# Kernel tuning notes

Measured on AMD Instinct MI355X. Metric: run time of the kernel, lower is better.

Reference implementation:

```python
import jax, jax.numpy as jnp
import numpy as np
from jax import lax

B, S, C, H, T = 64, 256, 64, 512, 128  # batch, enc seq, coord_dims, hidden, target_len

def _lstm_step(Wih, Whh, b, h, c, xt):
    # PyTorch gate order: i, f, g, o
    g = xt @ Wih.T + h @ Whh.T + b
    i, f, gg, o = jnp.split(g, 4, axis=-1)
    i = jax.nn.sigmoid(i); f = jax.nn.sigmoid(f)
    gg = jnp.tanh(gg); o = jax.nn.sigmoid(o)
    c = f * c + i * gg
    h = o * jnp.tanh(c)
    return h, c

def _lstm_layer(x_seq, Wih, Whh, b):
    # x_seq: [B, S, D] -> outputs [B, S, H], final (h, c)
    Bsz = x_seq.shape[0]
    h0 = jnp.zeros((Bsz, Whh.shape[1]), x_seq.dtype)
    c0 = jnp.zeros_like(h0)
    def step(carry, xt):
        h, c = carry
        h, c = _lstm_step(Wih, Whh, b, h, c, xt)
        return (h, c), h
    (hT, cT), ys = lax.scan(step, (h0, c0), x_seq.swapaxes(0, 1))
    return ys.swapaxes(0, 1), hT, cT

def setup_inputs() -> dict:
    key = jax.random.key(0)
    ks = jax.random.split(key, 16)
    s = 1.0 / np.sqrt(H)
    def u(k, shape):
        return jax.random.uniform(k, shape, jnp.float32, -s, s)
    inp = {"x": jax.random.normal(ks[0], (B, S, C), jnp.float32), "target_len": T}
    inp["enc_Wih0"] = u(ks[1], (4 * H, C)); inp["enc_Whh0"] = u(ks[2], (4 * H, H)); inp["enc_b0"] = u(ks[3], (4 * H,))
    inp["enc_Wih1"] = u(ks[4], (4 * H, H)); inp["enc_Whh1"] = u(ks[5], (4 * H, H)); inp["enc_b1"] = u(ks[6], (4 * H,))
    inp["dec_Wih0"] = u(ks[7], (4 * H, C)); inp["dec_Whh0"] = u(ks[8], (4 * H, H)); inp["dec_b0"] = u(ks[9], (4 * H,))
    inp["dec_Wih1"] = u(ks[10], (4 * H, H)); inp["dec_Whh1"] = u(ks[11], (4 * H, H)); inp["dec_b1"] = u(ks[12], (4 * H,))
    inp["lin_W"] = u(ks[13], (C, H)); inp["lin_b"] = u(ks[14], (C,))
    return inp

def reference(x, enc_Wih0, enc_Whh0, enc_b0, enc_Wih1, enc_Whh1, enc_b1,
              dec_Wih0, dec_Whh0, dec_b0, dec_Wih1, dec_Whh1, dec_b1,
              lin_W, lin_b, target_len):
    # ---- encoder: 2-layer LSTM over full sequence ----
    y0, h0, c0 = _lstm_layer(x, enc_Wih0, enc_Whh0, enc_b0)
    _, h1, c1 = _lstm_layer(y0, enc_Wih1, enc_Whh1, enc_b1)
    dec_in0 = x[:, -1, :]  # [B, C]
    def step(carry, _):
        xin, h0_, c0_, h1_, c1_ = carry
        h0n, c0n = _lstm_step(dec_Wih0, dec_Whh0, dec_b0, h0_, c0_, xin)
        h1n, c1n = _lstm_step(dec_Wih1, dec_Whh1, dec_b1, h1_, c1_, h0n)
        out = h1n @ lin_W.T + lin_b  # [B, C]
        return (out, h0n, c0n, h1n, c1n), out
    _, outs = lax.scan(step, (dec_in0, h0, c0, h1, c1), None, length=target_len)
    return outs.swapaxes(0, 1)  # [B, target_len, C]
```

## Files before the change

kernel.cpp:

```cpp
#include <hip/hip_runtime.h>

typedef _Float16 f16;
typedef _Float16 f16x4 __attribute__((ext_vector_type(4)));
typedef _Float16 f16x8 __attribute__((ext_vector_type(8)));
typedef float    f32x4 __attribute__((ext_vector_type(4)));

#define MFMA16(a,b,c) __builtin_amdgcn_mfma_f32_16x16x32_f16((a),(b),(c),0,0,0)

constexpr unsigned NB = 64, NS = 256, NC = 64, NH = 512, NT = 128;
constexpr unsigned HSLOT = NB * NH;

constexpr unsigned OFF_WX   = 0;
constexpr unsigned OFF_WLIN = OFF_WX   + NB*NS*NC*2;
constexpr unsigned OFF_EH0  = OFF_WLIN + NC*NH*2;
constexpr unsigned OFF_EH1  = OFF_EH0  + 2*HSLOT*2;
constexpr unsigned OFF_DH0  = OFF_EH1  + 2*HSLOT*2;
constexpr unsigned OFF_DH1  = OFF_DH0  + 2*HSLOT*2;
constexpr unsigned OFF_BAR  = OFF_DH1  + 2*HSLOT*2;


__global__ void prep_convert(const float* __restrict__ x,
                             const float* __restrict__ linw,
                             char* __restrict__ ws)
{
    unsigned rel = blockIdx.x * 256u + threadIdx.x;
    if (rel < 65536u) {
        unsigned t = rel >> 8, c4 = (rel >> 4) & 15u, b0 = (rel & 15u) << 2;
        #pragma unroll
        for (unsigned j = 0; j < 4; ++j) {
            float4 v = ((const float4*)x)[(b0 + j) * 4096u + t * 16u + c4];
            f16x4 o; o[0]=(f16)v.x; o[1]=(f16)v.y; o[2]=(f16)v.z; o[3]=(f16)v.w;
            ((f16x4*)(ws + OFF_WX))[t * 1024u + c4 * 64u + b0 + j] = o;
        }
    } else if ((rel -= 65536u) < 8192u) {
        float4 v = ((const float4*)linw)[rel];
        f16x4 o; o[0]=(f16)v.x; o[1]=(f16)v.y; o[2]=(f16)v.z; o[3]=(f16)v.w;
        ((f16x4*)(ws + OFF_WLIN))[rel] = o;
    } else if ((rel -= 8192u) < 32768u) {
        f16x8 z = {};
        ((f16x8*)(ws + OFF_EH0))[rel] = z;
    } else if ((rel -= 32768u) < 512u) {
        int4 z; z.x = z.y = z.z = z.w = 0;
        ((int4*)(ws + OFF_BAR))[rel] = z;
    }
}


__device__ __forceinline__ float sigm(float v)   { return 1.f / (1.f + __expf(-v)); }
__device__ __forceinline__ float tanh_f(float v) { return 2.f / (1.f + __expf(-2.f * v)) - 1.f; }

__device__ __forceinline__ void h_store8(f16* p, f16x4 v)
{
    union { unsigned long long u; f16x4 h; } c; c.h = v;
    __hip_atomic_store((unsigned long long*)p, c.u, __ATOMIC_RELAXED, __HIP_MEMORY_SCOPE_AGENT);
}
__device__ __forceinline__ f16x4 h_load8(const f16* p)
{
    unsigned long long v = __hip_atomic_load((const unsigned long long*)p,
                                             __ATOMIC_RELAXED, __HIP_MEMORY_SCOPE_AGENT);
    union { unsigned long long u; f16x4 h; } c; c.u = v;
    return c.h;
}
__device__ __forceinline__ f16x8 h_load_blk(const f16* slot, int kr, int m)
{
    const f16* p = slot + ((kr >> 2) << 8) + (m << 2);
    f16x4 a = h_load8(p);
    f16x4 b = h_load8(p + 256);
    f16x8 r;
    r[0]=a[0]; r[1]=a[1]; r[2]=a[2]; r[3]=a[3];
    r[4]=b[0]; r[5]=b[1]; r[6]=b[2]; r[7]=b[3];
    return r;
}

__device__ __forceinline__ void grid_barrier(int* bar, int wg, int tid, int& bgen)
{
    __syncthreads();
    if (tid == 0) {
        const int g = wg >> 4;
        int* grp   = bar + g * 32;
        int* root  = bar + 16 * 32;
        int* flags = bar + 17 * 32;
        const int target = bgen + 1;

        int old = __hip_atomic_fetch_add(grp, 1, __ATOMIC_RELAXED, __HIP_MEMORY_SCOPE_AGENT);
        if ((old & 15) == 15) {
            int ro = __hip_atomic_fetch_add(root, 1, __ATOMIC_RELAXED, __HIP_MEMORY_SCOPE_AGENT);
            if ((ro & 15) == 15) {
                #pragma unroll
                for (int i = 0; i < 16; ++i)
                    __hip_atomic_store(flags + i * 32, target, __ATOMIC_RELAXED, __HIP_MEMORY_SCOPE_AGENT);
            }
        }
        int* myf = flags + g * 32;
        while (__hip_atomic_load(myf, __ATOMIC_RELAXED, __HIP_MEMORY_SCOPE_AGENT) < target)
            __builtin_amdgcn_s_sleep(1);
        bgen = target;
    }
    __syncthreads();
}

__device__ __forceinline__ void load_wlds_f32(f16 (*Wlds)[1032],
                                              const float* __restrict__ A, int KA,
                                              const float* __restrict__ Bs, int KB,
                                              int u0, int tid)
{
    int nch = (KA + KB) >> 2;
    int tot = nch << 6;
    for (int idx = tid; idx < tot; idx += 256) {
        int j = idx / nch, ch = idx - j * nch;
        int k = ch << 2;
        int grow = ((j >> 4) << 9) + u0 + (j & 15);
        float4 v;
        if (k < KA) v = *(const float4*)(A + grow * KA + k);
        else        v = *(const float4*)(Bs + grow * KB + (k - KA));
        f16x4 o; o[0]=(f16)v.x; o[1]=(f16)v.y; o[2]=(f16)v.z; o[3]=(f16)v.w;
        *(f16x4*)&Wlds[j][k] = o;
    }
}

__device__ __forceinline__ void load_wlds_fold(f16 (*Wlds)[1032],
                                               const float* __restrict__ dwih0,
                                               const float* __restrict__ linw,
                                               const float* __restrict__ dwhh0,
                                               int u0, int tid)
{
    #pragma unroll
    for (int rep = 0; rep < 4; ++rep) {
        int idx = ((rep << 8) + tid) << 5;
        int j = idx >> 9, k0 = idx & 511;
        int grow = ((j >> 4) << 9) + u0 + (j & 15);
        float acc[32];
        #pragma unroll
        for (int q = 0; q < 32; ++q) acc[q] = 0.f;
        for (int c = 0; c < 64; ++c) {
            float wc = dwih0[grow * 64 + c];
            const float* lr = linw + c * 512 + k0;
            #pragma unroll
            for (int q = 0; q < 32; ++q) acc[q] += wc * lr[q];
        }
        #pragma unroll
        for (int q = 0; q < 32; ++q) Wlds[j][k0 + q] = (f16)acc[q];
    }
    int tot = 8192;
    for (int idx = tid; idx < tot; idx += 256) {
        int j = idx >> 7, ch = idx & 127, k = ch << 2;
        int grow = ((j >> 4) << 9) + u0 + (j & 15);
        float4 v = *(const float4*)(dwhh0 + grow * 512 + k);
        f16x4 o; o[0]=(f16)v.x; o[1]=(f16)v.y; o[2]=(f16)v.z; o[3]=(f16)v.w;
        *(f16x4*)&Wlds[j][512 + k] = o;
    }
}

template<int MAXS, bool EXACT>
__device__ __forceinline__ void rnn_round(f16 (*Wlds)[1032], float (*Dp)[16][68],
                                          const f16* __restrict__ A0, int K0,
                                          const f16* __restrict__ A1,
                                          int K, int kStart,
                                          const float* ba, float& creg,
                                          f16* __restrict__ ho,
                                          int u0, int b0, int tid)
{
    const int lane = tid & 63, wv = tid >> 6, q = lane >> 4, lo = lane & 15;
    const int sBeg = kStart >> 5, n = (K >> 5) - sBeg;
    const int per = n >> 2, rem = n & 3;
    const int s0 = sBeg + wv * per + (wv < rem ? wv : rem);
    const int ns = EXACT ? MAXS : (per + (wv < rem ? 1 : 0));

    int sEff[MAXS];
    #pragma unroll
    for (int s = 0; s < MAXS; ++s)
        sEff[s] = s0 + (EXACT ? s : (s < ns ? s : ns - 1));

    f16x8 A[MAXS];
    #pragma unroll
    for (int s = 0; s < MAXS; ++s) {
        int kb = sEff[s] << 5;
        bool in0 = kb < K0;
        const f16* src = in0 ? A0 : A1;
        int kr = (in0 ? kb : kb - K0) + (q << 3);
        A[s] = h_load_blk(src, kr, b0 + lo);
    }
    if (!EXACT) {
        if (MAXS - 1 >= ns) { f16x8 z = {}; A[MAXS-1] = z; }
    }
    __builtin_amdgcn_sched_barrier(0);

    f32x4 ac0 = {0.f,0.f,0.f,0.f}, ac1 = ac0, ac2 = ac0, ac3 = ac0;
    #pragma unroll
    for (int s = 0; s < MAXS; ++s) {
        int kk = (sEff[s] << 5) + (q << 3);
        ac0 = MFMA16(A[s], *(const f16x8*)&Wlds[lo     ][kk], ac0);
        ac1 = MFMA16(A[s], *(const f16x8*)&Wlds[lo + 16][kk], ac1);
        ac2 = MFMA16(A[s], *(const f16x8*)&Wlds[lo + 32][kk], ac2);
        ac3 = MFMA16(A[s], *(const f16x8*)&Wlds[lo + 48][kk], ac3);
    }

    #pragma unroll
    for (int r = 0; r < 4; ++r) {
        int rr = (q << 2) + r;
        Dp[wv][rr][lo     ] = ac0[r];
        Dp[wv][rr][lo + 16] = ac1[r];
        Dp[wv][rr][lo + 32] = ac2[r];
        Dp[wv][rr][lo + 48] = ac3[r];
    }
    __syncthreads();
    const int b = tid >> 4, u = tid & 15;
    float v[4];
    #pragma unroll
    for (int g = 0; g < 4; ++g) {
        int col = (g << 4) + u;
        v[g] = Dp[0][b][col] + Dp[1][b][col] + Dp[2][b][col] + Dp[3][b][col] + ba[g];
    }
    float ii = sigm(v[0]), ff = sigm(v[1]), gg = tanh_f(v[2]), oo = sigm(v[3]);
    creg = ff * creg + ii * gg;
    float h = oo * tanh_f(creg);
    float h1 = __shfl_down(h, 1);
    float h2 = __shfl_down(h, 2);
    float h3 = __shfl_down(h, 3);
    if ((u & 3) == 0) {
        f16x4 hv; hv[0] = (f16)h; hv[1] = (f16)h1; hv[2] = (f16)h2; hv[3] = (f16)h3;
        h_store8(ho + (((u0 + u) >> 2) << 8) + ((b0 + b) << 2), hv);
    }
}

__device__ __forceinline__ void out_gemm(const f16* __restrict__ H1,
                                         const f16* __restrict__ LW,
                                         const float* __restrict__ linb,
                                         float* __restrict__ out,
                                         int w, int t, int tid)
{
    const int lane = tid & 63, wv = tid >> 6, q = lane >> 4, lo = lane & 15;
    int b0 = w << 4;
    f32x4 ac = {0.f,0.f,0.f,0.f};
    int c0 = wv << 4;

    f16x8 a[16];
    #pragma unroll
    for (int s = 0; s < 16; ++s)
        a[s] = h_load_blk(H1, (s << 5) + (q << 3), b0 + lo);
    __builtin_amdgcn_sched_barrier(0);

    #pragma unroll
    for (int s = 0; s < 16; ++s) {
        int kk = (s << 5) + (q << 3);
        f16x8 bf = *(const f16x8*)(LW + (c0 + lo) * 512 + kk);
        ac = MFMA16(a[s], bf, ac);
    }
    float lb = linb[c0 + lo];
    #pragma unroll
    for (int r = 0; r < 4; ++r) {
        int b = b0 + (q << 2) + r;
        out[(size_t)b * (NT * NC) + t * NC + c0 + lo] = ac[r] + lb;
    }
}


__global__ void __launch_bounds__(256)
lstm_main(char* __restrict__ ws,
          const float* __restrict__ x,
          const float* __restrict__ wih0, const float* __restrict__ whh0, const float* __restrict__ eb0,
          const float* __restrict__ wih1, const float* __restrict__ whh1, const float* __restrict__ eb1,
          const float* __restrict__ dwih0, const float* __restrict__ dwhh0, const float* __restrict__ db0,
          const float* __restrict__ dwih1, const float* __restrict__ dwhh1, const float* __restrict__ db1,
          const float* __restrict__ linw, const float* __restrict__ linb,
          float* __restrict__ out)
{
    __shared__ f16   Wlds[64][1032];
    __shared__ float Dp[4][16][68];

    const int wg = blockIdx.x, tid = threadIdx.x;
    const bool isL0 = wg < 128;
    const int wl = wg & 127;
    const int b0 = (wl & 3) << 4;
    const int u0 = (wl >> 2) << 4;
    const int u  = tid & 15;
    int* bar = (int*)(ws + OFF_BAR);
    int bgen = 0;

    const f16* WX   = (const f16*)(ws + OFF_WX);
    const f16* WLIN = (const f16*)(ws + OFF_WLIN);
    f16* EH0 = (f16*)(ws + OFF_EH0);
    f16* EH1 = (f16*)(ws + OFF_EH1);
    f16* DH0 = (f16*)(ws + OFF_DH0);
    f16* DH1 = (f16*)(ws + OFF_DH1);

    if (isL0) load_wlds_f32(Wlds, wih0,  64, whh0, 512, u0, tid);
    else      load_wlds_f32(Wlds, wih1, 512, whh1, 512, u0, tid);
    __syncthreads();

    float ba[4];
    {
        const float* bs = isL0 ? eb0 : eb1;
        #pragma unroll
        for (int g = 0; g < 4; ++g) ba[g] = bs[(g << 9) + u0 + u];
    }
    float creg = 0.f;

    for (int r = 0; r <= (int)NS; ++r) {
        if (isL0 && r < (int)NS) {
            rnn_round<5,false>(Wlds, Dp,
                      WX + r * 4096, 64,
                      EH0 + ((r + 1) & 1) * HSLOT,
                      576, 0, ba, creg,
                      EH0 + (r & 1) * HSLOT, u0, b0, tid);
        } else if (!isL0 && r >= 1) {
            int t = r - 1;
            rnn_round<8,true>(Wlds, Dp,
                      EH0 + (t & 1) * HSLOT, 512,
                      EH1 + ((t + 1) & 1) * HSLOT,
                      1024, 0, ba, creg,
                      EH1 + (t & 1) * HSLOT, u0, b0, tid);
        }
        grid_barrier(bar, wg, tid, bgen);
    }

    float baI[4];
    if (isL0) {
        load_wlds_fold(Wlds, dwih0, linw, dwhh0, u0, tid);
        const int bb = b0 + (tid >> 4);
        const float* xr = x + bb * (NS * NC) + (NS - 1) * NC;
        #pragma unroll
        for (int g = 0; g < 4; ++g) {
            int row = (g << 9) + u0 + u;
            const float* wr = dwih0 + row * 64;
            float bsum = 0.f, xsum = 0.f;
            for (int c = 0; c < 64; ++c) { bsum += linb[c] * wr[c]; xsum += xr[c] * wr[c]; }
            ba[g]  = db0[row] + bsum;
            baI[g] = db0[row] + xsum;
        }
    } else {
        load_wlds_f32(Wlds, dwih1, 512, dwhh1, 512, u0, tid);
        #pragma unroll
        for (int g = 0; g < 4; ++g) { ba[g] = db1[(g << 9) + u0 + u]; baI[g] = 0.f; }
    }
    __syncthreads();

    for (int d = 0; d < 2 * (int)NT; ++d) {
        int t = d >> 1;
        if ((d & 1) == 0) {
            if (isL0) {
                if (t == 0) {
                    rnn_round<4,true>(Wlds, Dp, EH1 + HSLOT, 512, EH0 + HSLOT,
                              1024, 512, baI, creg,
                              DH0, u0, b0, tid);
                } else {
                    rnn_round<8,true>(Wlds, Dp,
                              DH1 + ((t + 1) & 1) * HSLOT, 512,
                              DH0 + ((t + 1) & 1) * HSLOT,
                              1024, 0, ba, creg,
                              DH0 + (t & 1) * HSLOT, u0, b0, tid);
                }
            } else if (wg < 132 && t >= 1) {
                out_gemm(DH1 + ((t - 1) & 1) * HSLOT, WLIN, linb, out, wg - 128, t - 1, tid);
            }
        } else {
            if (!isL0) {
                const f16* A1 = (t == 0) ? EH1 + HSLOT : DH1 + ((t + 1) & 1) * HSLOT;
                rnn_round<8,true>(Wlds, Dp,
                          DH0 + (t & 1) * HSLOT, 512,
                          A1, 1024, 0, ba, creg,
                          DH1 + (t & 1) * HSLOT, u0, b0, tid);
            }
        }
        grid_barrier(bar, wg, tid, bgen);
    }

    if (!isL0 && wg < 132)
        out_gemm(DH1 + HSLOT, WLIN, linb, out, wg - 128, (int)NT - 1, tid);
}


extern "C" void kernel_launch(void* const* d_in, const int* in_sizes, int n_in,
                              void* d_out, int out_size, void* d_ws, size_t ws_size,
                              hipStream_t stream)
{
    const float* x     = (const float*)d_in[0];
    const float* wih0  = (const float*)d_in[2];
    const float* whh0  = (const float*)d_in[3];
    const float* eb0   = (const float*)d_in[4];
    const float* wih1  = (const float*)d_in[5];
    const float* whh1  = (const float*)d_in[6];
    const float* eb1   = (const float*)d_in[7];
    const float* dwih0 = (const float*)d_in[8];
    const float* dwhh0 = (const float*)d_in[9];
    const float* db0   = (const float*)d_in[10];
    const float* dwih1 = (const float*)d_in[11];
    const float* dwhh1 = (const float*)d_in[12];
    const float* db1   = (const float*)d_in[13];
    const float* linw  = (const float*)d_in[14];
    const float* linb  = (const float*)d_in[15];
    char* ws    = (char*)d_ws;
    float* outp = (float*)d_out;

    prep_convert<<<418, 256, 0, stream>>>(x, linw, ws);

    lstm_main<<<256, 256, 0, stream>>>(ws, x, wih0, whh0, eb0, wih1, whh1, eb1,
                                       dwih0, dwhh0, db0, dwih1, dwhh1, db1,
                                       linw, linb, outp);
}
```

Before: 2.110 ms.

## Precompute recurrent-half GEMM during idle phase to shorten critical path

Each layer's workgroups now compute the half of the gate GEMM that depends on their own recurrent state (Whh·h) during the phase when they would otherwise idle. The partial accumulators are carried in registers to the next phase. That phase then only does the half that depends on the other layer's fresh output before the activation. This halves the MFMA work on the critical path between grid barriers. It costs extra register pressure and work in the previously idle phase, which for layer-1 groups now overlaps with the output GEMM.

```diff
diff --git a/kernel.cpp b/kernel.cpp
--- a/kernel.cpp
+++ b/kernel.cpp
@@ -151,50 +151,37 @@
     }
 }
 
-template<int MAXS, bool EXACT>
-__device__ __forceinline__ void rnn_round(f16 (*Wlds)[1032], float (*Dp)[16][68],
-                                          const f16* __restrict__ A0, int K0,
-                                          const f16* __restrict__ A1,
-                                          int K, int kStart,
-                                          const float* ba, float& creg,
-                                          f16* __restrict__ ho,
-                                          int u0, int b0, int tid)
+__device__ __forceinline__ void gemm_acc4(f16 (*Wlds)[1032],
+                                          const f16* __restrict__ A0, int kOff,
+                                          f32x4& ac0, f32x4& ac1, f32x4& ac2, f32x4& ac3,
+                                          int b0, int tid)
 {
     const int lane = tid & 63, wv = tid >> 6, q = lane >> 4, lo = lane & 15;
-    const int sBeg = kStart >> 5, n = (K >> 5) - sBeg;
-    const int per = n >> 2, rem = n & 3;
-    const int s0 = sBeg + wv * per + (wv < rem ? wv : rem);
-    const int ns = EXACT ? MAXS : (per + (wv < rem ? 1 : 0));
-
-    int sEff[MAXS];
-    #pragma unroll
-    for (int s = 0; s < MAXS; ++s)
-        sEff[s] = s0 + (EXACT ? s : (s < ns ? s : ns - 1));
-
-    f16x8 A[MAXS];
-    #pragma unroll
-    for (int s = 0; s < MAXS; ++s) {
-        int kb = sEff[s] << 5;
-        bool in0 = kb < K0;
-        const f16* src = in0 ? A0 : A1;
-        int kr = (in0 ? kb : kb - K0) + (q << 3);
-        A[s] = h_load_blk(src, kr, b0 + lo);
-    }
-    if (!EXACT) {
-        if (MAXS - 1 >= ns) { f16x8 z = {}; A[MAXS-1] = z; }
+    const int s0 = wv << 2;
+    f16x8 A[4];
+    #pragma unroll
+    for (int s = 0; s < 4; ++s) {
+        int kr = ((s0 + s) << 5) + (q << 3);
+        A[s] = h_load_blk(A0, kr, b0 + lo);
     }
     __builtin_amdgcn_sched_barrier(0);
-
-    f32x4 ac0 = {0.f,0.f,0.f,0.f}, ac1 = ac0, ac2 = ac0, ac3 = ac0;
-    #pragma unroll
-    for (int s = 0; s < MAXS; ++s) {
-        int kk = (sEff[s] << 5) + (q << 3);
+    #pragma unroll
+    for (int s = 0; s < 4; ++s) {
+        int kk = kOff + ((s0 + s) << 5) + (q << 3);
         ac0 = MFMA16(A[s], *(const f16x8*)&Wlds[lo     ][kk], ac0);
         ac1 = MFMA16(A[s], *(const f16x8*)&Wlds[lo + 16][kk], ac1);
         ac2 = MFMA16(A[s], *(const f16x8*)&Wlds[lo + 32][kk], ac2);
         ac3 = MFMA16(A[s], *(const f16x8*)&Wlds[lo + 48][kk], ac3);
     }
-
+}
+
+__device__ __forceinline__ void finish_round(float (*Dp)[16][68],
+                                             f32x4 ac0, f32x4 ac1, f32x4 ac2, f32x4 ac3,
+                                             const float* ba, float& creg,
+                                             f16* __restrict__ ho,
+                                             int u0, int b0, int tid)
+{
+    const int lane = tid & 63, wv = tid >> 6, q = lane >> 4, lo = lane & 15;
     #pragma unroll
     for (int r = 0; r < 4; ++r) {
         int rr = (q << 2) + r;
@@ -221,6 +208,52 @@
         f16x4 hv; hv[0] = (f16)h; hv[1] = (f16)h1; hv[2] = (f16)h2; hv[3] = (f16)h3;
         h_store8(ho + (((u0 + u) >> 2) << 8) + ((b0 + b) << 2), hv);
     }
+}
+
+template<int MAXS, bool EXACT>
+__device__ __forceinline__ void rnn_round(f16 (*Wlds)[1032], float (*Dp)[16][68],
+                                          const f16* __restrict__ A0, int K0,
+                                          const f16* __restrict__ A1,
+                                          int K, int kStart,
+                                          const float* ba, float& creg,
+                                          f16* __restrict__ ho,
+                                          int u0, int b0, int tid)
+{
+    const int lane = tid & 63, wv = tid >> 6, q = lane >> 4, lo = lane & 15;
+    const int sBeg = kStart >> 5, n = (K >> 5) - sBeg;
+    const int per = n >> 2, rem = n & 3;
+    const int s0 = sBeg + wv * per + (wv < rem ? wv : rem);
+    const int ns = EXACT ? MAXS : (per + (wv < rem ? 1 : 0));
+
+    int sEff[MAXS];
+    #pragma unroll
+    for (int s = 0; s < MAXS; ++s)
+        sEff[s] = s0 + (EXACT ? s : (s < ns ? s : ns - 1));
+
+    f16x8 A[MAXS];
+    #pragma unroll
+    for (int s = 0; s < MAXS; ++s) {
+        int kb = sEff[s] << 5;
+        bool in0 = kb < K0;
+        const f16* src = in0 ? A0 : A1;
+        int kr = (in0 ? kb : kb - K0) + (q << 3);
+        A[s] = h_load_blk(src, kr, b0 + lo);
+    }
+    if (!EXACT) {
+        if (MAXS - 1 >= ns) { f16x8 z = {}; A[MAXS-1] = z; }
+    }
+    __builtin_amdgcn_sched_barrier(0);
+
+    f32x4 ac0 = {0.f,0.f,0.f,0.f}, ac1 = ac0, ac2 = ac0, ac3 = ac0;
+    #pragma unroll
+    for (int s = 0; s < MAXS; ++s) {
+        int kk = (sEff[s] << 5) + (q << 3);
+        ac0 = MFMA16(A[s], *(const f16x8*)&Wlds[lo     ][kk], ac0);
+        ac1 = MFMA16(A[s], *(const f16x8*)&Wlds[lo + 16][kk], ac1);
+        ac2 = MFMA16(A[s], *(const f16x8*)&Wlds[lo + 32][kk], ac2);
+        ac3 = MFMA16(A[s], *(const f16x8*)&Wlds[lo + 48][kk], ac3);
+    }
+    finish_round(Dp, ac0, ac1, ac2, ac3, ba, creg, ho, u0, b0, tid);
 }
 
 __device__ __forceinline__ void out_gemm(const f16* __restrict__ H1,
@@ -335,31 +368,39 @@
     }
     __syncthreads();
 
+    f32x4 c0 = {0.f,0.f,0.f,0.f}, c1 = c0, c2 = c0, c3 = c0;
+    const f32x4 zero = {0.f,0.f,0.f,0.f};
+
     for (int d = 0; d < 2 * (int)NT; ++d) {
         int t = d >> 1;
         if ((d & 1) == 0) {
             if (isL0) {
                 if (t == 0) {
-                    rnn_round<4,true>(Wlds, Dp, EH1 + HSLOT, 512, EH0 + HSLOT,
-                              1024, 512, baI, creg,
-                              DH0, u0, b0, tid);
+                    f32x4 a0 = zero, a1 = zero, a2 = zero, a3 = zero;
+                    gemm_acc4(Wlds, EH0 + HSLOT, 512, a0, a1, a2, a3, b0, tid);
+                    finish_round(Dp, a0, a1, a2, a3, baI, creg, DH0, u0, b0, tid);
                 } else {
-                    rnn_round<8,true>(Wlds, Dp,
-                              DH1 + ((t + 1) & 1) * HSLOT, 512,
-                              DH0 + ((t + 1) & 1) * HSLOT,
-                              1024, 0, ba, creg,
-                              DH0 + (t & 1) * HSLOT, u0, b0, tid);
+                    f32x4 a0 = c0, a1 = c1, a2 = c2, a3 = c3;
+                    gemm_acc4(Wlds, DH1 + ((t + 1) & 1) * HSLOT, 0, a0, a1, a2, a3, b0, tid);
+                    finish_round(Dp, a0, a1, a2, a3, ba, creg,
+                                 DH0 + (t & 1) * HSLOT, u0, b0, tid);
                 }
-            } else if (wg < 132 && t >= 1) {
-                out_gemm(DH1 + ((t - 1) & 1) * HSLOT, WLIN, linb, out, wg - 128, t - 1, tid);
+            } else {
+                const f16* h1p = (t == 0) ? EH1 + HSLOT : DH1 + ((t + 1) & 1) * HSLOT;
+                c0 = zero; c1 = zero; c2 = zero; c3 = zero;
+                gemm_acc4(Wlds, h1p, 512, c0, c1, c2, c3, b0, tid);
+                if (wg < 132 && t >= 1)
+                    out_gemm(DH1 + ((t - 1) & 1) * HSLOT, WLIN, linb, out, wg - 128, t - 1, tid);
             }
         } else {
             if (!isL0) {
-                const f16* A1 = (t == 0) ? EH1 + HSLOT : DH1 + ((t + 1) & 1) * HSLOT;
-                rnn_round<8,true>(Wlds, Dp,
-                          DH0 + (t & 1) * HSLOT, 512,
-                          A1, 1024, 0, ba, creg,
-                          DH1 + (t & 1) * HSLOT, u0, b0, tid);
+                f32x4 a0 = c0, a1 = c1, a2 = c2, a3 = c3;
+                gemm_acc4(Wlds, DH0 + (t & 1) * HSLOT, 0, a0, a1, a2, a3, b0, tid);
+                finish_round(Dp, a0, a1, a2, a3, ba, creg,
+                             DH1 + (t & 1) * HSLOT, u0, b0, tid);
+            } else if (t < (int)NT - 1) {
+                c0 = zero; c1 = zero; c2 = zero; c3 = zero;
+                gemm_acc4(Wlds, DH0 + (t & 1) * HSLOT, 512, c0, c1, c2, c3, b0, tid);
             }
         }
         grid_barrier(bar, wg, tid, bgen);
```

After: 2.092 ms. About the same (-0.8%).
